# Performance work log

Measured on AMD Instinct MI355X. Metric: run time of the kernel, lower is better.

## Reference

```python
import jax, jax.numpy as jnp
import numpy as np

N_NODES, N_EDGES, N_GRAPHS = 20000, 640000, 256
D_IN, H1, H2, H3, L, H4, ED = 7, 128, 128, 64, 16, 64, 1


def _gat_conv(x, src, dst, edge_attr, W, att_s, att_d, We, att_e, b):
    """PyG GATConv (heads=1, concat=True, edge_dim=ED, add_self_loops=True,
    fill_value='mean' for self-loop edge attrs, negative_slope=0.2)."""
    n = x.shape[0]
    h = x @ W                                  # [N, F]
    a_s = h @ att_s                            # [N]
    a_d = h @ att_d                            # [N]
    # append self loops; self-loop edge attr = mean of edge attrs
    loop = jnp.arange(n)
    src_f = jnp.concatenate([src, loop])
    dst_f = jnp.concatenate([dst, loop])
    ea_mean = edge_attr.mean(axis=0, keepdims=True)
    ea = jnp.concatenate([edge_attr, jnp.broadcast_to(ea_mean, (n, edge_attr.shape[1]))], axis=0)
    a_e = (ea @ We) @ att_e                    # [E+N]
    logits = jax.nn.leaky_relu(a_s[src_f] + a_d[dst_f] + a_e, 0.2)
    # neighborhood softmax over incoming edges of each dst node
    m = jax.ops.segment_max(logits, dst_f, num_segments=n)
    ex = jnp.exp(logits - m[dst_f])
    denom = jax.ops.segment_sum(ex, dst_f, num_segments=n)
    alpha = ex / denom[dst_f]                  # [E+N]
    out = jax.ops.segment_sum(alpha[:, None] * h[src_f], dst_f, num_segments=n)
    return out + b


def _branch(x, edge_index, edge_col, params):
    src, dst = edge_index[0], edge_index[1]
    for p in params:  # fixed 3 layers
        x = jax.nn.elu(_gat_conv(x, src, dst, edge_col, *p))
        # dropout p=0.2 is identity in eval mode
    return x


def _mean_pool(x, batch, num_graphs):
    s = jax.ops.segment_sum(x, batch, num_segments=num_graphs)
    cnt = jax.ops.segment_sum(jnp.ones((x.shape[0],), x.dtype), batch, num_segments=num_graphs)
    return s / jnp.maximum(cnt, 1.0)[:, None]


def setup_inputs() -> dict:
    key = jax.random.key(0)
    ks = jax.random.split(key, 40)
    inp = {
        "x1": jax.random.normal(ks[0], (N_NODES, D_IN), jnp.float32),
        "x2": jax.random.normal(ks[1], (N_NODES, D_IN), jnp.float32),
        "edge_index1": jax.random.randint(ks[2], (2, N_EDGES), 0, N_NODES),
        "edge_index2": jax.random.randint(ks[3], (2, N_EDGES), 0, N_NODES),
        "batch1": jnp.sort(jax.random.randint(ks[4], (N_NODES,), 0, N_GRAPHS)),
        "batch2": jnp.sort(jax.random.randint(ks[5], (N_NODES,), 0, N_GRAPHS)),
        "x_norm2_1": jax.random.normal(ks[6], (N_GRAPHS, L), jnp.float32),
        "x_norm2_2": jax.random.normal(ks[7], (N_GRAPHS, L), jnp.float32),
        "edge_col1": jax.random.normal(ks[8], (N_EDGES, ED), jnp.float32),
        "edge_col2": jax.random.normal(ks[9], (N_EDGES, ED), jnp.float32),
    }
    dims = [(D_IN, H1), (H1, H2), (H2, H3)]
    k = 10
    for i, (fi, fo) in enumerate(dims, start=1):
        sc = 1.0 / np.sqrt(fi)
        inp[f"W{i}"] = jax.random.normal(ks[k], (fi, fo), jnp.float32) * sc; k += 1
        inp[f"as{i}"] = jax.random.normal(ks[k], (fo,), jnp.float32) * 0.1; k += 1
        inp[f"ad{i}"] = jax.random.normal(ks[k], (fo,), jnp.float32) * 0.1; k += 1
        inp[f"We{i}"] = jax.random.normal(ks[k], (ED, fo), jnp.float32); k += 1
        inp[f"ae{i}"] = jax.random.normal(ks[k], (fo,), jnp.float32) * 0.1; k += 1
        inp[f"b{i}"] = jnp.zeros((fo,), jnp.float32); k += 1
    inp["linW"] = jax.random.normal(ks[k], (H3 + L, H4), jnp.float32) * (1.0 / np.sqrt(H3 + L)); k += 1
    inp["linb"] = jnp.zeros((H4,), jnp.float32)
    return inp


def reference(x1, x2, edge_index1, edge_index2, batch1, batch2, x_norm2_1, x_norm2_2,
              edge_col1, edge_col2,
              W1, as1, ad1, We1, ae1, b1,
              W2, as2, ad2, We2, ae2, b2,
              W3, as3, ad3, We3, ae3, b3,
              linW, linb):
    params = [(W1, as1, ad1, We1, ae1, b1),
              (W2, as2, ad2, We2, ae2, b2),
              (W3, as3, ad3, We3, ae3, b3)]
    h1 = _branch(x1, edge_index1, edge_col1, params)
    h2 = _branch(x2, edge_index2, edge_col2, params)
    g1 = _mean_pool(h1, batch1, N_GRAPHS)
    g2 = _mean_pool(h2, batch2, N_GRAPHS)
    o1 = jnp.concatenate([g1, x_norm2_1], axis=1) @ linW + linb
    o2 = jnp.concatenate([g2, x_norm2_2], axis=1) @ linW + linb
    return (o1, o2)
```

## Files before the change

### kernel.cpp

```cpp
#include <hip/hip_runtime.h>
#include <hip/hip_bf16.h>
#include <hip/hip_fp16.h>

#define N_NODES 20000
#define N_EDGES 640000
#define N_GRAPHS 256
#define NBUCK 313
#define NC 160
#define EPC 4000
#define DCAP 2560
#define CURP 16
#define STAGEN ((size_t)NBUCK*DCAP)

typedef short bf16v __attribute__((ext_vector_type(8)));
typedef float f32x4 __attribute__((ext_vector_type(4)));
typedef float f32x2 __attribute__((ext_vector_type(2)));

__device__ __forceinline__ float leaky02(float x){ return x > 0.f ? x : 0.2f*x; }
__device__ __forceinline__ float eluf(float x){ return x > 0.f ? x : (__expf(x) - 1.f); }
__device__ __forceinline__ unsigned short f2bf(float x){
  __hip_bfloat16 t = __float2bfloat16(x);
  return *reinterpret_cast<unsigned short*>(&t);
}
__device__ __forceinline__ float bflo(unsigned int u){ return __uint_as_float(u << 16); }
__device__ __forceinline__ float bfhi(unsigned int u){ return __uint_as_float(u & 0xffff0000u); }
__device__ __forceinline__ float bfs(unsigned short u){ return __uint_as_float(((unsigned)u) << 16); }
__device__ __forceinline__ void pkfma(f32x2& acc, f32x2 a, f32x2 b){
  asm volatile("v_pk_fma_f32 %0, %1, %2, %0" : "+v"(acc) : "v"(a), "v"(b));
}

__global__ __launch_bounds__(512) void setup_kernel(
    const int* __restrict__ bat0, const int* __restrict__ bat1,
    const float* __restrict__ We1, const float* __restrict__ ae1,
    const float* __restrict__ We2, const float* __restrict__ ae2,
    const float* __restrict__ We3, const float* __restrict__ ae3,
    int* __restrict__ bcur, int* __restrict__ gb, float* __restrict__ scal)
{
  int b = blockIdx.x;
  int tid = threadIdx.x;
  if (tid < NBUCK) bcur[((size_t)b*NBUCK + tid)*CURP] = tid*DCAP;
  {
    const int* batch = b ? bat1 : bat0;
    int* gbb = gb + b*257;
    if (tid <= N_GRAPHS){
      int g = tid, lo = 0, hi = N_NODES;
      while (lo < hi){ int mid = (lo+hi) >> 1; if (batch[mid] < g) lo = mid+1; else hi = mid; }
      gbb[g] = lo;
    }
  }
  if (b == 0){
    int wv = tid >> 6, lane = tid & 63;
    if (wv < 3){
      const float* We = wv==0 ? We1 : (wv==1 ? We2 : We3);
      const float* ae = wv==0 ? ae1 : (wv==1 ? ae2 : ae3);
      int F = (wv==2) ? 64 : 128;
      float s = 0.f;
      for (int i = lane; i < F; i += 64) s += We[i]*ae[i];
      for (int o = 32; o; o >>= 1) s += __shfl_down(s, o);
      if (lane == 0) scal[2+wv] = s;
    }
  }
}

__global__ __launch_bounds__(256) void binC_kernel(
    const int* __restrict__ ei0, const int* __restrict__ ei1,
    const float* __restrict__ ec0, const float* __restrict__ ec1,
    int* __restrict__ bcur, uint2* __restrict__ stage, float* __restrict__ part)
{
  int b = blockIdx.y;
  const int* srcp = (b ? ei1 : ei0);
  const int* dstp = srcp + N_EDGES;
  const float* ec = b ? ec1 : ec0;
  int* bcurb = bcur + (size_t)b*NBUCK*CURP;
  uint2* stageb = stage + (size_t)b*STAGEN;
  __shared__ uint2 recs[EPC];
  __shared__ int hist[NBUCK], rbase[NBUCK], rcur[NBUCK];
  int tid = threadIdx.x;
  for (int j = tid; j < NBUCK; j += 256){ hist[j] = 0; rcur[j] = 0; }
  __syncthreads();
  int e0 = blockIdx.x*EPC;
  float v = 0.f;
  for (int r = tid; r < EPC; r += 256){
    int i = e0 + r;
    int d = dstp[i];
    int bk = d >> 6;
    uint2 rec;
    rec.x = (unsigned)srcp[i] | ((unsigned)(d & 63) << 16);
    float e = ec[i];
    v += e;
    rec.y = ((unsigned)f2bf(e) << 16) | (unsigned)bk;
    recs[r] = rec;
    atomicAdd(&hist[bk], 1);
  }
  __syncthreads();
  for (int j = tid; j < NBUCK; j += 256){
    int h = hist[j];
    rbase[j] = h ? atomicAdd(&bcurb[j*CURP], h) : 0;
  }
  __syncthreads();
  for (int r = tid; r < EPC; r += 256){
    uint2 rc = recs[r];
    int bk = (int)(rc.y & 0xFFFFu);
    int p = rbase[bk] + atomicAdd(&rcur[bk], 1);
    if (p < (bk + 1)*DCAP) stageb[p] = rc;
  }
  for (int o = 32; o; o >>= 1) v += __shfl_down(v, o);
  __shared__ float wr[4];
  int lane = tid & 63, wv = tid >> 6;
  if (lane == 0) wr[wv] = v;
  __syncthreads();
  if (tid == 0) part[b*NC + blockIdx.x] = wr[0]+wr[1]+wr[2]+wr[3];
}

__global__ __launch_bounds__(256) void binD_kernel(
    const uint2* __restrict__ stage, const int* __restrict__ bcur,
    const float* __restrict__ part,
    unsigned* __restrict__ final_, int2* __restrict__ rowp2, float* __restrict__ scal)
{
  int b = blockIdx.y;
  int g = blockIdx.x;
  int tid = threadIdx.x;
  if (g == 0){
    float s = 0.f;
    for (int i = tid; i < NC; i += 256) s += part[b*NC + i];
    for (int o = 32; o; o >>= 1) s += __shfl_down(s, o);
    __shared__ float fr[4];
    if ((tid & 63) == 0) fr[tid >> 6] = s;
    __syncthreads();
    if (tid == 0) scal[b] = fr[0]+fr[1]+fr[2]+fr[3];
  }
  const uint2* stageb = stage + (size_t)b*STAGEN;
  unsigned* finb = final_ + (size_t)b*STAGEN;
  int2* rowb = rowp2 + (size_t)b*N_NODES;
  int cb = g*DCAP;
  int n = min(bcur[((size_t)b*NBUCK + g)*CURP] - cb, DCAP);
  __shared__ uint2 recs[DCAP];
  __shared__ int cnt64[64], cur64[64], off64[64];
  if (tid < 64) cnt64[tid] = 0;
  __syncthreads();
  for (int r = tid; r < n; r += 256){
    uint2 rc = stageb[cb + r];
    recs[r] = rc;
    atomicAdd(&cnt64[(rc.x >> 16) & 63], 1);
  }
  __syncthreads();
  if (tid == 0){
    int acc = 0;
    for (int dl = 0; dl < 64; ++dl){
      off64[dl] = acc; cur64[dl] = acc; acc += cnt64[dl];
    }
  }
  __syncthreads();
  int nd = min(64, N_NODES - g*64);
  if (tid < nd)
    rowb[g*64 + tid] = make_int2(cb + off64[tid], cb + off64[tid] + cnt64[tid]);
  for (int r = tid; r < n; r += 256){
    uint2 rc = recs[r];
    int dl = (rc.x >> 16) & 63;
    int p = atomicAdd(&cur64[dl], 1);
    finb[cb + p] = (rc.y & 0xFFFF0000u) | (rc.x & 0xFFFFu);
  }
}

template<int K, int F>
__global__ __launch_bounds__(256) void node_linear1_kernel(
    const float* __restrict__ x0, const float* __restrict__ x1,
    const float* __restrict__ W,
    const float* __restrict__ atts, const float* __restrict__ attd,
    unsigned short* __restrict__ hbAll, float* __restrict__ aSAll, float* __restrict__ aDAll)
{
  int b = blockIdx.y;
  const float* x = b ? x1 : x0;
  unsigned short* hb = hbAll + (size_t)b*N_NODES*128;
  float* a_s = aSAll + b*N_NODES;
  float* a_d = aDAll + b*N_NODES;
  constexpr int ROWS = 256 / F;
  __shared__ float Wl[K*F];
  __shared__ float xl[ROWS*K];
  __shared__ float swv[4], dwv[4];
  int tid = threadIdx.x;
  for (int i = tid; i < K*F; i += 256) Wl[i] = W[i];
  int f = tid % F;
  int lr = tid / F;
  float vs = atts[f], vd = attd[f];
  const int ntiles = (N_NODES + ROWS - 1)/ROWS;
  for (int t = blockIdx.x; t < ntiles; t += gridDim.x){
    int r0 = t*ROWS;
    __syncthreads();
    for (int i = tid; i < ROWS*K; i += 256){
      int r = i / K, k = i % K;
      int row = r0 + r;
      xl[i] = (row < N_NODES) ? x[row*K + k] : 0.f;
    }
    __syncthreads();
    float acc = 0.f;
    #pragma unroll
    for (int k = 0; k < K; ++k) acc += xl[lr*K + k] * Wl[k*F + f];
    int row = r0 + lr;
    if (row < N_NODES) hb[row*F + f] = f2bf(acc);
    float s = acc*vs, d = acc*vd;
    #pragma unroll
    for (int o = 32; o; o >>= 1){ s += __shfl_down(s, o); d += __shfl_down(d, o); }
    int wv = tid >> 6;
    if ((tid & 63) == 0){ swv[wv] = s; dwv[wv] = d; }
    __syncthreads();
    if (f == 0 && row < N_NODES){
      a_s[row] = swv[2*lr] + swv[2*lr+1];
      a_d[row] = dwv[2*lr] + dwv[2*lr+1];
    }
  }
}

template<int F>
__global__ __launch_bounds__(256) void gemm_mfma_kernel(
    const unsigned short* __restrict__ AAll, const float* __restrict__ W,
    const float* __restrict__ atts, const float* __restrict__ attd,
    unsigned short* __restrict__ hbAll, float* __restrict__ aSAll, float* __restrict__ aDAll)
{
  int b = blockIdx.y;
  const unsigned short* A = AAll + (size_t)b*N_NODES*128;
  unsigned short* hb = hbAll + (size_t)b*N_NODES*128;
  float* a_s = aSAll + b*N_NODES;
  float* a_d = aDAll + b*N_NODES;
  constexpr int NT = F/16;
  constexpr int KP = 136;
  __shared__ unsigned short Wb[F*KP];
  int tid = threadIdx.x;
  for (int idx = tid; idx < 128*F; idx += 256){
    int k = idx / F, col = idx % F;
    Wb[col*KP + k] = f2bf(W[idx]);
  }
  __syncthreads();
  int wave = tid >> 6, lane = tid & 63;
  int r0w = blockIdx.x*64 + wave*16;
  int arow = r0w + (lane & 15);
  bool av = arow < N_NODES;
  f32x4 acc[NT];
  #pragma unroll
  for (int nt = 0; nt < NT; ++nt) acc[nt] = 0.f;
  #pragma unroll
  for (int step = 0; step < 4; ++step){
    int kbase = step*32 + (lane>>4)*8;
    uint4 araw = av ? *reinterpret_cast<const uint4*>(&A[(size_t)arow*128 + kbase])
                    : make_uint4(0,0,0,0);
    bf16v af = __builtin_bit_cast(bf16v, araw);
    #pragma unroll
    for (int nt = 0; nt < NT; ++nt){
      uint4 braw = *reinterpret_cast<const uint4*>(&Wb[(nt*16 + (lane&15))*KP + kbase]);
      bf16v bfr = __builtin_bit_cast(bf16v, braw);
      acc[nt] = __builtin_amdgcn_mfma_f32_16x16x32_bf16(af, bfr, acc[nt], 0, 0, 0);
    }
  }
  float ps[4] = {0,0,0,0}, pd[4] = {0,0,0,0};
  #pragma unroll
  for (int nt = 0; nt < NT; ++nt){
    int col = nt*16 + (lane&15);
    float vs = atts[col], vd = attd[col];
    #pragma unroll
    for (int reg = 0; reg < 4; ++reg){
      int row = r0w + (lane>>4)*4 + reg;
      float v = acc[nt][reg];
      if (row < N_NODES) hb[(size_t)row*F + col] = f2bf(v);
      ps[reg] += v*vs;
      pd[reg] += v*vd;
    }
  }
  #pragma unroll
  for (int reg = 0; reg < 4; ++reg){
    float s = ps[reg], d = pd[reg];
    #pragma unroll
    for (int o = 1; o < 16; o <<= 1){ s += __shfl_xor(s, o); d += __shfl_xor(d, o); }
    int row = r0w + (lane>>4)*4 + reg;
    if ((lane & 15) == 0 && row < N_NODES){ a_s[row] = s; a_d[row] = d; }
  }
}

template<int F>
__global__ __launch_bounds__(256) void aggregate_kernel(
    const unsigned short* __restrict__ hbAll,
    const float* __restrict__ aSAll, const float* __restrict__ aDAll,
    const unsigned* __restrict__ edgAll, const int2* __restrict__ rowp2All,
    const float* __restrict__ scal, int l,
    const float* __restrict__ bias,
    unsigned short* __restrict__ outbAll)
{
  constexpr int PERL = F/16;
  constexpr int PERH = PERL/2;
  constexpr int RSH = (F == 128) ? 8 : 7;
  constexpr int SUBB = (F == 128) ? 16 : 8;
  int bid = blockIdx.x;
  int b = bid & 1;
  const unsigned short* hb = hbAll + (size_t)b*N_NODES*128;
  const float* a_s = aSAll + b*N_NODES;
  const float* a_d = aDAll + b*N_NODES;
  const unsigned* edges = edgAll + (size_t)b*STAGEN;
  const int2* rowp2 = rowp2All + (size_t)b*N_NODES;
  __shared__ uint2 sp[4][64];
  int wv = threadIdx.x >> 6;
  int lane = threadIdx.x & 63;
  int half = lane >> 5;
  int hl = lane & 31;
  int d = (bid >> 1)*8 + wv*2 + half;
  int sub = hl & 15, grp = hl >> 4;
  const char* hb2 = (const char*)hb + sub*SUBB;
  float c = scal[2+l];
  float ae_self = (scal[b] * (1.0f/N_EDGES)) * c;
  float add_ = a_d[d];
  float p_self = __expf(fminf(leaky02(a_s[d] + add_ + ae_self), 60.f));
  float dsum = 0.f;
  f32x2 acc[PERH];
  #pragma unroll
  for (int i = 0; i < PERH; ++i) acc[i] = (f32x2){0.f, 0.f};
  if (grp == 0){
    f32x2 pself2 = {p_self, p_self};
    if (PERL == 8){
      uint4 q = *reinterpret_cast<const uint4*>(hb2 + ((unsigned)d << RSH));
      pkfma(acc[0], (f32x2){bflo(q.x), bfhi(q.x)}, pself2);
      pkfma(acc[1], (f32x2){bflo(q.y), bfhi(q.y)}, pself2);
      pkfma(acc[2], (f32x2){bflo(q.z), bfhi(q.z)}, pself2);
      pkfma(acc[3], (f32x2){bflo(q.w), bfhi(q.w)}, pself2);
    } else {
      uint2 q = *reinterpret_cast<const uint2*>(hb2 + ((unsigned)d << RSH));
      pkfma(acc[0], (f32x2){bflo(q.x), bfhi(q.x)}, pself2);
      pkfma(acc[1], (f32x2){bflo(q.y), bfhi(q.y)}, pself2);
    }
  }
  int2 r2 = rowp2[d];
  int e0 = r2.x, deg = r2.y - r2.x;
  int degmax = max(deg, __shfl_xor(deg, 32));
  const int cap = (int)STAGEN - 1;
  unsigned eRec = edges[min(e0 + hl, cap)];
  for (int ch = 0; ch < degmax; ch += 32){
    int n = deg - ch;
    unsigned eNext = edges[min(e0 + ch + 32 + hl, cap)];
    unsigned s0 = eRec & 0xFFFFu;
    float aval = a_s[s0];
    unsigned off0 = 0;
    float p0 = 0.f;
    if (hl < n){
      p0 = __expf(fminf(leaky02(aval + add_ + c*bfhi(eRec)), 60.f));
      off0 = s0 << RSH;
    }
    dsum += p0;
    sp[wv][lane] = make_uint2(off0, __float_as_uint(p0));
    int nmax = min(32, degmax - ch);
    #pragma unroll 4
    for (int e8 = 0; e8 < nmax; e8 += 8){
      int base = half*32 + e8 + grp;
      uint2 r0 = sp[wv][base];
      uint2 r1 = sp[wv][base + 2];
      uint2 rr2 = sp[wv][base + 4];
      uint2 r3 = sp[wv][base + 6];
      f32x2 a0 = {__uint_as_float(r0.y), __uint_as_float(r0.y)};
      f32x2 a1 = {__uint_as_float(r1.y), __uint_as_float(r1.y)};
      f32x2 a2 = {__uint_as_float(rr2.y), __uint_as_float(rr2.y)};
      f32x2 a3 = {__uint_as_float(r3.y), __uint_as_float(r3.y)};
      if (PERL == 8){
        uint4 q0 = *reinterpret_cast<const uint4*>(hb2 + r0.x);
        uint4 q1 = *reinterpret_cast<const uint4*>(hb2 + r1.x);
        uint4 q2 = *reinterpret_cast<const uint4*>(hb2 + rr2.x);
        uint4 q3 = *reinterpret_cast<const uint4*>(hb2 + r3.x);
        pkfma(acc[0], (f32x2){bflo(q0.x), bfhi(q0.x)}, a0);
        pkfma(acc[1], (f32x2){bflo(q0.y), bfhi(q0.y)}, a0);
        pkfma(acc[2], (f32x2){bflo(q0.z), bfhi(q0.z)}, a0);
        pkfma(acc[3], (f32x2){bflo(q0.w), bfhi(q0.w)}, a0);
        pkfma(acc[0], (f32x2){bflo(q1.x), bfhi(q1.x)}, a1);
        pkfma(acc[1], (f32x2){bflo(q1.y), bfhi(q1.y)}, a1);
        pkfma(acc[2], (f32x2){bflo(q1.z), bfhi(q1.z)}, a1);
        pkfma(acc[3], (f32x2){bflo(q1.w), bfhi(q1.w)}, a1);
        pkfma(acc[0], (f32x2){bflo(q2.x), bfhi(q2.x)}, a2);
        pkfma(acc[1], (f32x2){bflo(q2.y), bfhi(q2.y)}, a2);
        pkfma(acc[2], (f32x2){bflo(q2.z), bfhi(q2.z)}, a2);
        pkfma(acc[3], (f32x2){bflo(q2.w), bfhi(q2.w)}, a2);
        pkfma(acc[0], (f32x2){bflo(q3.x), bfhi(q3.x)}, a3);
        pkfma(acc[1], (f32x2){bflo(q3.y), bfhi(q3.y)}, a3);
        pkfma(acc[2], (f32x2){bflo(q3.z), bfhi(q3.z)}, a3);
        pkfma(acc[3], (f32x2){bflo(q3.w), bfhi(q3.w)}, a3);
      } else {
        uint2 q0 = *reinterpret_cast<const uint2*>(hb2 + r0.x);
        uint2 q1 = *reinterpret_cast<const uint2*>(hb2 + r1.x);
        uint2 q2 = *reinterpret_cast<const uint2*>(hb2 + rr2.x);
        uint2 q3 = *reinterpret_cast<const uint2*>(hb2 + r3.x);
        pkfma(acc[0], (f32x2){bflo(q0.x), bfhi(q0.x)}, a0);
        pkfma(acc[1], (f32x2){bflo(q0.y), bfhi(q0.y)}, a0);
        pkfma(acc[0], (f32x2){bflo(q1.x), bfhi(q1.x)}, a1);
        pkfma(acc[1], (f32x2){bflo(q1.y), bfhi(q1.y)}, a1);
        pkfma(acc[0], (f32x2){bflo(q2.x), bfhi(q2.x)}, a2);
        pkfma(acc[1], (f32x2){bflo(q2.y), bfhi(q2.y)}, a2);
        pkfma(acc[0], (f32x2){bflo(q3.x), bfhi(q3.x)}, a3);
        pkfma(acc[1], (f32x2){bflo(q3.y), bfhi(q3.y)}, a3);
      }
    }
    eRec = eNext;
  }
  #pragma unroll
  for (int o = 16; o; o >>= 1) dsum += __shfl_xor(dsum, o);
  float denom = p_self + dsum;
  float inv = 1.0f/denom;
  float vv[PERL];
  #pragma unroll
  for (int i = 0; i < PERH; ++i){
    float v0 = acc[i].x, v1 = acc[i].y;
    v0 += __shfl_xor(v0, 16);
    v1 += __shfl_xor(v1, 16);
    vv[2*i]   = eluf(v0*inv + bias[PERL*sub + 2*i]);
    vv[2*i+1] = eluf(v1*inv + bias[PERL*sub + 2*i+1]);
  }
  if (grp == 0){
    unsigned short* outb = outbAll + (size_t)b*N_NODES*F;
    if (PERL == 8){
      uint4 o;
      o.x = (unsigned int)f2bf(vv[0]) | ((unsigned int)f2bf(vv[1]) << 16);
      o.y = (unsigned int)f2bf(vv[2]) | ((unsigned int)f2bf(vv[3]) << 16);
      o.z = (unsigned int)f2bf(vv[4]) | ((unsigned int)f2bf(vv[5]) << 16);
      o.w = (unsigned int)f2bf(vv[6]) | ((unsigned int)f2bf(vv[7]) << 16);
      *reinterpret_cast<uint4*>(&outb[(size_t)d*F + 8*sub]) = o;
    } else {
      uint2 o;
      o.x = (unsigned int)f2bf(vv[0]) | ((unsigned int)f2bf(vv[1]) << 16);
      o.y = (unsigned int)f2bf(vv[2]) | ((unsigned int)f2bf(vv[3]) << 16);
      *reinterpret_cast<uint2*>(&outb[(size_t)d*F + 4*sub]) = o;
    }
  }
}

__global__ __launch_bounds__(256) void pool_final_kernel(
    const unsigned short* __restrict__ buf, const int* __restrict__ gb,
    const float* __restrict__ xn0, const float* __restrict__ xn1,
    const float* __restrict__ linW, const float* __restrict__ linb,
    float* __restrict__ out)
{
  int bg = blockIdx.x;
  int b = bg >> 8, g = bg & 255;
  __shared__ float Wl[80*64];
  __shared__ float red[4][64];
  __shared__ float mf[64];
  int tid = threadIdx.x;
  for (int i = tid; i < 80*64; i += 256) Wl[i] = linW[i];
  const unsigned short* x = buf + (size_t)b*N_NODES*64;
  const int* gbb = gb + b*257;
  int s = gbb[g], e = gbb[g+1];
  int f = tid & 63, rg = tid >> 6;
  float acc = 0.f;
  for (int r = s + rg; r < e; r += 4) acc += bfs(x[(size_t)r*64 + f]);
  red[rg][f] = acc;
  __syncthreads();
  if (rg == 0)
    mf[f] = (red[0][f]+red[1][f]+red[2][f]+red[3][f]) / fmaxf((float)(e - s), 1.0f);
  __syncthreads();
  if (tid < 64){
    int j = tid;
    const float* xn = b ? xn1 : xn0;
    float a2 = linb[j];
    #pragma unroll 8
    for (int k = 0; k < 64; ++k) a2 += mf[k] * Wl[k*64 + j];
    #pragma unroll
    for (int k = 0; k < 16; ++k) a2 += xn[g*16+k] * Wl[(64+k)*64 + j];
    out[(size_t)(b*N_GRAPHS + g)*64 + j] = a2;
  }
}

extern "C" void kernel_launch(void* const* d_in, const int* in_sizes, int n_in,
                              void* d_out, int out_size, void* d_ws, size_t ws_size,
                              hipStream_t stream)
{
  const float* x1   = (const float*)d_in[0];
  const float* x2   = (const float*)d_in[1];
  const int*   ei1  = (const int*)d_in[2];
  const int*   ei2  = (const int*)d_in[3];
  const int*   bat1 = (const int*)d_in[4];
  const int*   bat2 = (const int*)d_in[5];
  const float* xn1  = (const float*)d_in[6];
  const float* xn2  = (const float*)d_in[7];
  const float* ec1  = (const float*)d_in[8];
  const float* ec2  = (const float*)d_in[9];
  const float* W[3]   = {(const float*)d_in[10], (const float*)d_in[16], (const float*)d_in[22]};
  const float* as_[3] = {(const float*)d_in[11], (const float*)d_in[17], (const float*)d_in[23]};
  const float* ad_[3] = {(const float*)d_in[12], (const float*)d_in[18], (const float*)d_in[24]};
  const float* We[3]  = {(const float*)d_in[13], (const float*)d_in[19], (const float*)d_in[25]};
  const float* ae[3]  = {(const float*)d_in[14], (const float*)d_in[20], (const float*)d_in[26]};
  const float* bb[3]  = {(const float*)d_in[15], (const float*)d_in[21], (const float*)d_in[27]};
  const float* linW = (const float*)d_in[28];
  const float* linb = (const float*)d_in[29];
  float* out = (float*)d_out;

  char* ws = (char*)d_ws;
  size_t off = 0;
  auto alloc = [&](size_t bytes)->char*{
    char* p = ws + off;
    off = (off + bytes + 255) & ~(size_t)255;
    return p;
  };
  unsigned short* hbA = (unsigned short*)alloc((size_t)2*N_NODES*128*2);
  unsigned short* hbB = (unsigned short*)alloc((size_t)2*N_NODES*128*2);
  float* aS   = (float*)alloc((size_t)2*N_NODES*4);
  float* aD   = (float*)alloc((size_t)2*N_NODES*4);
  int* bcur   = (int*)alloc((size_t)2*NBUCK*CURP*4);
  int2* rowp2 = (int2*)alloc((size_t)2*N_NODES*8);
  uint2* stage = (uint2*)alloc((size_t)2*STAGEN*8);
  unsigned* final_ = (unsigned*)alloc((size_t)2*STAGEN*4);
  float* part = (float*)alloc((size_t)2*NC*4);
  int* gb     = (int*)alloc((size_t)2*257*4);
  float* scal = (float*)alloc(64);

  setup_kernel<<<2, 512, 0, stream>>>(bat1, bat2,
      We[0], ae[0], We[1], ae[1], We[2], ae[2], bcur, gb, scal);
  binC_kernel<<<dim3(NC,2), 256, 0, stream>>>(ei1, ei2, ec1, ec2, bcur, stage, part);
  binD_kernel<<<dim3(NBUCK,2), 256, 0, stream>>>(stage, bcur, part, final_, rowp2, scal);

  const int AGG = 2*(N_NODES/8);

  node_linear1_kernel<7,128><<<dim3(1024,2), 256, 0, stream>>>(
      x1, x2, W[0], as_[0], ad_[0], hbA, aS, aD);
  aggregate_kernel<128><<<AGG, 256, 0, stream>>>(
      hbA, aS, aD, final_, rowp2, scal, 0, bb[0], hbB);

  gemm_mfma_kernel<128><<<dim3((N_NODES+63)/64,2), 256, 0, stream>>>(
      hbB, W[1], as_[1], ad_[1], hbA, aS, aD);
  aggregate_kernel<128><<<AGG, 256, 0, stream>>>(
      hbA, aS, aD, final_, rowp2, scal, 1, bb[1], hbB);

  gemm_mfma_kernel<64><<<dim3((N_NODES+63)/64,2), 256, 0, stream>>>(
      hbB, W[2], as_[2], ad_[2], hbA, aS, aD);
  aggregate_kernel<64><<<AGG, 256, 0, stream>>>(
      hbA, aS, aD, final_, rowp2, scal, 2, bb[2], hbB);

  pool_final_kernel<<<2*N_GRAPHS, 256, 0, stream>>>(
      hbB, gb, xn1, xn2, linW, linb, out);
}
```

Before: 180.8 us.

## Split 128-wide feature tables into two 64-wide halves aggregated separately

```diff
diff --git a/kernel.cpp b/kernel.cpp
--- a/kernel.cpp
+++ b/kernel.cpp
@@ -11,6 +11,7 @@
 #define DCAP 2560
 #define CURP 16
 #define STAGEN ((size_t)NBUCK*DCAP)
+#define LOG2E 1.44269504f
 
 typedef short bf16v __attribute__((ext_vector_type(8)));
 typedef float f32x4 __attribute__((ext_vector_type(4)));
@@ -167,11 +168,13 @@
     const float* __restrict__ x0, const float* __restrict__ x1,
     const float* __restrict__ W,
     const float* __restrict__ atts, const float* __restrict__ attd,
-    unsigned short* __restrict__ hbAll, float* __restrict__ aSAll, float* __restrict__ aDAll)
+    unsigned short* __restrict__ loAll, unsigned short* __restrict__ hiAll,
+    float* __restrict__ aSAll, float* __restrict__ aDAll)
 {
   int b = blockIdx.y;
   const float* x = b ? x1 : x0;
-  unsigned short* hb = hbAll + (size_t)b*N_NODES*128;
+  unsigned short* lo = loAll + (size_t)b*N_NODES*64;
+  unsigned short* hi = hiAll + (size_t)b*N_NODES*64;
   float* a_s = aSAll + b*N_NODES;
   float* a_d = aDAll + b*N_NODES;
   constexpr int ROWS = 256 / F;
@@ -197,7 +200,10 @@
     #pragma unroll
     for (int k = 0; k < K; ++k) acc += xl[lr*K + k] * Wl[k*F + f];
     int row = r0 + lr;
-    if (row < N_NODES) hb[row*F + f] = f2bf(acc);
+    if (row < N_NODES){
+      if (f < 64) lo[(size_t)row*64 + f] = f2bf(acc);
+      else        hi[(size_t)row*64 + f - 64] = f2bf(acc);
+    }
     float s = acc*vs, d = acc*vd;
     #pragma unroll
     for (int o = 32; o; o >>= 1){ s += __shfl_down(s, o); d += __shfl_down(d, o); }
@@ -205,8 +211,8 @@
     if ((tid & 63) == 0){ swv[wv] = s; dwv[wv] = d; }
     __syncthreads();
     if (f == 0 && row < N_NODES){
-      a_s[row] = swv[2*lr] + swv[2*lr+1];
-      a_d[row] = dwv[2*lr] + dwv[2*lr+1];
+      a_s[row] = (swv[2*lr] + swv[2*lr+1])*LOG2E;
+      a_d[row] = (dwv[2*lr] + dwv[2*lr+1])*LOG2E;
     }
   }
 }
@@ -215,11 +221,13 @@
 __global__ __launch_bounds__(256) void gemm_mfma_kernel(
     const unsigned short* __restrict__ AAll, const float* __restrict__ W,
     const float* __restrict__ atts, const float* __restrict__ attd,
-    unsigned short* __restrict__ hbAll, float* __restrict__ aSAll, float* __restrict__ aDAll)
+    unsigned short* __restrict__ OloAll, unsigned short* __restrict__ OhiAll,
+    float* __restrict__ aSAll, float* __restrict__ aDAll)
 {
   int b = blockIdx.y;
   const unsigned short* A = AAll + (size_t)b*N_NODES*128;
-  unsigned short* hb = hbAll + (size_t)b*N_NODES*128;
+  unsigned short* Olo = OloAll + (size_t)b*N_NODES*64;
+  unsigned short* Ohi = (F == 128) ? (OhiAll + (size_t)b*N_NODES*64) : nullptr;
   float* a_s = aSAll + b*N_NODES;
   float* a_d = aDAll + b*N_NODES;
   constexpr int NT = F/16;
@@ -256,11 +264,13 @@
   for (int nt = 0; nt < NT; ++nt){
     int col = nt*16 + (lane&15);
     float vs = atts[col], vd = attd[col];
+    unsigned short* O = (F == 64 || nt < 4) ? Olo : Ohi;
+    int co = (F == 64 || nt < 4) ? col : col - 64;
     #pragma unroll
     for (int reg = 0; reg < 4; ++reg){
       int row = r0w + (lane>>4)*4 + reg;
       float v = acc[nt][reg];
-      if (row < N_NODES) hb[(size_t)row*F + col] = f2bf(v);
+      if (row < N_NODES) O[(size_t)row*64 + co] = f2bf(v);
       ps[reg] += v*vs;
       pd[reg] += v*vd;
     }
@@ -271,26 +281,24 @@
     #pragma unroll
     for (int o = 1; o < 16; o <<= 1){ s += __shfl_xor(s, o); d += __shfl_xor(d, o); }
     int row = r0w + (lane>>4)*4 + reg;
-    if ((lane & 15) == 0 && row < N_NODES){ a_s[row] = s; a_d[row] = d; }
-  }
-}
-
-template<int F>
+    if ((lane & 15) == 0 && row < N_NODES){ a_s[row] = s*LOG2E; a_d[row] = d*LOG2E; }
+  }
+}
+
+template<int OUTS, bool SPLIT>
 __global__ __launch_bounds__(256) void aggregate_kernel(
-    const unsigned short* __restrict__ hbAll,
+    const unsigned short* __restrict__ tabLoAll, const unsigned short* __restrict__ tabHiAll,
     const float* __restrict__ aSAll, const float* __restrict__ aDAll,
     const unsigned* __restrict__ edgAll, const int2* __restrict__ rowp2All,
     const float* __restrict__ scal, int l,
     const float* __restrict__ bias,
     unsigned short* __restrict__ outbAll)
 {
-  constexpr int PERL = F/16;
-  constexpr int PERH = PERL/2;
-  constexpr int RSH = (F == 128) ? 8 : 7;
-  constexpr int SUBB = (F == 128) ? 16 : 8;
   int bid = blockIdx.x;
   int b = bid & 1;
-  const unsigned short* hb = hbAll + (size_t)b*N_NODES*128;
+  int hf = SPLIT ? ((bid >> 1) & 1) : 0;
+  int grpidx = SPLIT ? (bid >> 2) : (bid >> 1);
+  const unsigned short* tab = ((SPLIT && hf) ? tabHiAll : tabLoAll) + (size_t)b*N_NODES*64;
   const float* a_s = aSAll + b*N_NODES;
   const float* a_d = aDAll + b*N_NODES;
   const unsigned* edges = edgAll + (size_t)b*STAGEN;
@@ -300,30 +308,22 @@
   int lane = threadIdx.x & 63;
   int half = lane >> 5;
   int hl = lane & 31;
-  int d = (bid >> 1)*8 + wv*2 + half;
+  int d = grpidx*8 + wv*2 + half;
   int sub = hl & 15, grp = hl >> 4;
-  const char* hb2 = (const char*)hb + sub*SUBB;
-  float c = scal[2+l];
+  const char* hb2 = (const char*)tab + sub*8;
+  float c = scal[2+l]*LOG2E;
   float ae_self = (scal[b] * (1.0f/N_EDGES)) * c;
   float add_ = a_d[d];
-  float p_self = __expf(fminf(leaky02(a_s[d] + add_ + ae_self), 60.f));
+  float p_self = exp2f(fminf(leaky02(a_s[d] + add_ + ae_self), 86.f));
   float dsum = 0.f;
-  f32x2 acc[PERH];
-  #pragma unroll
-  for (int i = 0; i < PERH; ++i) acc[i] = (f32x2){0.f, 0.f};
+  f32x2 acc[2];
+  acc[0] = (f32x2){0.f, 0.f};
+  acc[1] = (f32x2){0.f, 0.f};
   if (grp == 0){
     f32x2 pself2 = {p_self, p_self};
-    if (PERL == 8){
-      uint4 q = *reinterpret_cast<const uint4*>(hb2 + ((unsigned)d << RSH));
-      pkfma(acc[0], (f32x2){bflo(q.x), bfhi(q.x)}, pself2);
-      pkfma(acc[1], (f32x2){bflo(q.y), bfhi(q.y)}, pself2);
-      pkfma(acc[2], (f32x2){bflo(q.z), bfhi(q.z)}, pself2);
-      pkfma(acc[3], (f32x2){bflo(q.w), bfhi(q.w)}, pself2);
-    } else {
-      uint2 q = *reinterpret_cast<const uint2*>(hb2 + ((unsigned)d << RSH));
-      pkfma(acc[0], (f32x2){bflo(q.x), bfhi(q.x)}, pself2);
-      pkfma(acc[1], (f32x2){bflo(q.y), bfhi(q.y)}, pself2);
-    }
+    uint2 q = *reinterpret_cast<const uint2*>(hb2 + ((unsigned)d << 7));
+    pkfma(acc[0], (f32x2){bflo(q.x), bfhi(q.x)}, pself2);
+    pkfma(acc[1], (f32x2){bflo(q.y), bfhi(q.y)}, pself2);
   }
   int2 r2 = rowp2[d];
   int e0 = r2.x, deg = r2.y - r2.x;
@@ -338,8 +338,8 @@
     unsigned off0 = 0;
     float p0 = 0.f;
     if (hl < n){
-      p0 = __expf(fminf(leaky02(aval + add_ + c*bfhi(eRec)), 60.f));
-      off0 = s0 << RSH;
+      p0 = exp2f(fminf(leaky02(aval + add_ + c*bfhi(eRec)), 86.f));
+      off0 = s0 << 7;
     }
     dsum += p0;
     sp[wv][lane] = make_uint2(off0, __float_as_uint(p0));
@@ -355,41 +355,18 @@
       f32x2 a1 = {__uint_as_float(r1.y), __uint_as_float(r1.y)};
       f32x2 a2 = {__uint_as_float(rr2.y), __uint_as_float(rr2.y)};
       f32x2 a3 = {__uint_as_float(r3.y), __uint_as_float(r3.y)};
-      if (PERL == 8){
-        uint4 q0 = *reinterpret_cast<const uint4*>(hb2 + r0.x);
-        uint4 q1 = *reinterpret_cast<const uint4*>(hb2 + r1.x);
-        uint4 q2 = *reinterpret_cast<const uint4*>(hb2 + rr2.x);
-        uint4 q3 = *reinterpret_cast<const uint4*>(hb2 + r3.x);
-        pkfma(acc[0], (f32x2){bflo(q0.x), bfhi(q0.x)}, a0);
-        pkfma(acc[1], (f32x2){bflo(q0.y), bfhi(q0.y)}, a0);
-        pkfma(acc[2], (f32x2){bflo(q0.z), bfhi(q0.z)}, a0);
-        pkfma(acc[3], (f32x2){bflo(q0.w), bfhi(q0.w)}, a0);
-        pkfma(acc[0], (f32x2){bflo(q1.x), bfhi(q1.x)}, a1);
-        pkfma(acc[1], (f32x2){bflo(q1.y), bfhi(q1.y)}, a1);
-        pkfma(acc[2], (f32x2){bflo(q1.z), bfhi(q1.z)}, a1);
-        pkfma(acc[3], (f32x2){bflo(q1.w), bfhi(q1.w)}, a1);
-        pkfma(acc[0], (f32x2){bflo(q2.x), bfhi(q2.x)}, a2);
-        pkfma(acc[1], (f32x2){bflo(q2.y), bfhi(q2.y)}, a2);
-        pkfma(acc[2], (f32x2){bflo(q2.z), bfhi(q2.z)}, a2);
-        pkfma(acc[3], (f32x2){bflo(q2.w), bfhi(q2.w)}, a2);
-        pkfma(acc[0], (f32x2){bflo(q3.x), bfhi(q3.x)}, a3);
-        pkfma(acc[1], (f32x2){bflo(q3.y), bfhi(q3.y)}, a3);
-        pkfma(acc[2], (f32x2){bflo(q3.z), bfhi(q3.z)}, a3);
-        pkfma(acc[3], (f32x2){bflo(q3.w), bfhi(q3.w)}, a3);
-      } else {
-        uint2 q0 = *reinterpret_cast<const uint2*>(hb2 + r0.x);
-        uint2 q1 = *reinterpret_cast<const uint2*>(hb2 + r1.x);
-        uint2 q2 = *reinterpret_cast<const uint2*>(hb2 + rr2.x);
-        uint2 q3 = *reinterpret_cast<const uint2*>(hb2 + r3.x);
-        pkfma(acc[0], (f32x2){bflo(q0.x), bfhi(q0.x)}, a0);
-        pkfma(acc[1], (f32x2){bflo(q0.y), bfhi(q0.y)}, a0);
-        pkfma(acc[0], (f32x2){bflo(q1.x), bfhi(q1.x)}, a1);
-        pkfma(acc[1], (f32x2){bflo(q1.y), bfhi(q1.y)}, a1);
-        pkfma(acc[0], (f32x2){bflo(q2.x), bfhi(q2.x)}, a2);
-        pkfma(acc[1], (f32x2){bflo(q2.y), bfhi(q2.y)}, a2);
-        pkfma(acc[0], (f32x2){bflo(q3.x), bfhi(q3.x)}, a3);
-        pkfma(acc[1], (f32x2){bflo(q3.y), bfhi(q3.y)}, a3);
-      }
+      uint2 q0 = *reinterpret_cast<const uint2*>(hb2 + r0.x);
+      uint2 q1 = *reinterpret_cast<const uint2*>(hb2 + r1.x);
+      uint2 q2 = *reinterpret_cast<const uint2*>(hb2 + rr2.x);
+      uint2 q3 = *reinterpret_cast<const uint2*>(hb2 + r3.x);
+      pkfma(acc[0], (f32x2){bflo(q0.x), bfhi(q0.x)}, a0);
+      pkfma(acc[1], (f32x2){bflo(q0.y), bfhi(q0.y)}, a0);
+      pkfma(acc[0], (f32x2){bflo(q1.x), bfhi(q1.x)}, a1);
+      pkfma(acc[1], (f32x2){bflo(q1.y), bfhi(q1.y)}, a1);
+      pkfma(acc[0], (f32x2){bflo(q2.x), bfhi(q2.x)}, a2);
+      pkfma(acc[1], (f32x2){bflo(q2.y), bfhi(q2.y)}, a2);
+      pkfma(acc[0], (f32x2){bflo(q3.x), bfhi(q3.x)}, a3);
+      pkfma(acc[1], (f32x2){bflo(q3.y), bfhi(q3.y)}, a3);
     }
     eRec = eNext;
   }
@@ -397,30 +374,21 @@
   for (int o = 16; o; o >>= 1) dsum += __shfl_xor(dsum, o);
   float denom = p_self + dsum;
   float inv = 1.0f/denom;
-  float vv[PERL];
+  float vv[4];
   #pragma unroll
-  for (int i = 0; i < PERH; ++i){
+  for (int i = 0; i < 2; ++i){
     float v0 = acc[i].x, v1 = acc[i].y;
     v0 += __shfl_xor(v0, 16);
     v1 += __shfl_xor(v1, 16);
-    vv[2*i]   = eluf(v0*inv + bias[PERL*sub + 2*i]);
-    vv[2*i+1] = eluf(v1*inv + bias[PERL*sub + 2*i+1]);
+    vv[2*i]   = eluf(v0*inv + bias[hf*64 + 4*sub + 2*i]);
+    vv[2*i+1] = eluf(v1*inv + bias[hf*64 + 4*sub + 2*i+1]);
   }
   if (grp == 0){
-    unsigned short* outb = outbAll + (size_t)b*N_NODES*F;
-    if (PERL == 8){
-      uint4 o;
-      o.x = (unsigned int)f2bf(vv[0]) | ((unsigned int)f2bf(vv[1]) << 16);
-      o.y = (unsigned int)f2bf(vv[2]) | ((unsigned int)f2bf(vv[3]) << 16);
-      o.z = (unsigned int)f2bf(vv[4]) | ((unsigned int)f2bf(vv[5]) << 16);
-      o.w = (unsigned int)f2bf(vv[6]) | ((unsigned int)f2bf(vv[7]) << 16);
-      *reinterpret_cast<uint4*>(&outb[(size_t)d*F + 8*sub]) = o;
-    } else {
-      uint2 o;
-      o.x = (unsigned int)f2bf(vv[0]) | ((unsigned int)f2bf(vv[1]) << 16);
-      o.y = (unsigned int)f2bf(vv[2]) | ((unsigned int)f2bf(vv[3]) << 16);
-      *reinterpret_cast<uint2*>(&outb[(size_t)d*F + 4*sub]) = o;
-    }
+    unsigned short* outb = outbAll + (size_t)b*N_NODES*OUTS;
+    uint2 o;
+    o.x = (unsigned int)f2bf(vv[0]) | ((unsigned int)f2bf(vv[1]) << 16);
+    o.y = (unsigned int)f2bf(vv[2]) | ((unsigned int)f2bf(vv[3]) << 16);
+    *reinterpret_cast<uint2*>(&outb[(size_t)d*OUTS + hf*64 + 4*sub]) = o;
   }
 }
 
@@ -491,8 +459,9 @@
     off = (off + bytes + 255) & ~(size_t)255;
     return p;
   };
-  unsigned short* hbA = (unsigned short*)alloc((size_t)2*N_NODES*128*2);
-  unsigned short* hbB = (unsigned short*)alloc((size_t)2*N_NODES*128*2);
+  unsigned short* tabLo = (unsigned short*)alloc((size_t)2*N_NODES*64*2);
+  unsigned short* tabHi = (unsigned short*)alloc((size_t)2*N_NODES*64*2);
+  unsigned short* hbU   = (unsigned short*)alloc((size_t)2*N_NODES*128*2);
   float* aS   = (float*)alloc((size_t)2*N_NODES*4);
   float* aD   = (float*)alloc((size_t)2*N_NODES*4);
   int* bcur   = (int*)alloc((size_t)2*NBUCK*CURP*4);
@@ -508,23 +477,24 @@
   binC_kernel<<<dim3(NC,2), 256, 0, stream>>>(ei1, ei2, ec1, ec2, bcur, stage, part);
   binD_kernel<<<dim3(NBUCK,2), 256, 0, stream>>>(stage, bcur, part, final_, rowp2, scal);
 
-  const int AGG = 2*(N_NODES/8);
+  const int AGG4 = 4*(N_NODES/8);
+  const int AGG2 = 2*(N_NODES/8);
 
   node_linear1_kernel<7,128><<<dim3(1024,2), 256, 0, stream>>>(
-      x1, x2, W[0], as_[0], ad_[0], hbA, aS, aD);
-  aggregate_kernel<128><<<AGG, 256, 0, stream>>>(
-      hbA, aS, aD, final_, rowp2, scal, 0, bb[0], hbB);
+      x1, x2, W[0], as_[0], ad_[0], tabLo, tabHi, aS, aD);
+  aggregate_kernel<128,true><<<AGG4, 256, 0, stream>>>(
+      tabLo, tabHi, aS, aD, final_, rowp2, scal, 0, bb[0], hbU);
 
   gemm_mfma_kernel<128><<<dim3((N_NODES+63)/64,2), 256, 0, stream>>>(
-      hbB, W[1], as_[1], ad_[1], hbA, aS, aD);
-  aggregate_kernel<128><<<AGG, 256, 0, stream>>>(
-      hbA, aS, aD, final_, rowp2, scal, 1, bb[1], hbB);
+      hbU, W[1], as_[1], ad_[1], tabLo, tabHi, aS, aD);
+  aggregate_kernel<128,true><<<AGG4, 256, 0, stream>>>(
+      tabLo, tabHi, aS, aD, final_, rowp2, scal, 1, bb[1], hbU);
 
   gemm_mfma_kernel<64><<<dim3((N_NODES+63)/64,2), 256, 0, stream>>>(
-      hbB, W[2], as_[2], ad_[2], hbA, aS, aD);
-  aggregate_kernel<64><<<AGG, 256, 0, stream>>>(
-      hbA, aS, aD, final_, rowp2, scal, 2, bb[2], hbB);
+      hbU, W[2], as_[2], ad_[2], tabLo, nullptr, aS, aD);
+  aggregate_kernel<64,false><<<AGG2, 256, 0, stream>>>(
+      tabLo, nullptr, aS, aD, final_, rowp2, scal, 2, bb[2], tabHi);
 
   pool_final_kernel<<<2*N_GRAPHS, 256, 0, stream>>>(
-      hbB, gb, xn1, xn2, linW, linb, out);
-}
+      tabHi, gb, xn1, xn2, linW, linb, out);
+}
```

Result: slower. 201.5 us (+11.4%).
